# Kernel optimization log

Measured on AMD Instinct MI355X. Metric: run time of the kernel, lower is better.

## Reference

```python
import jax, jax.numpy as jnp
import numpy as np
import math

DIM = 2048
N_HEADS = 16
HEAD_DIM = 128
BATCH = 2
T = 2048
EPS = 1e-5


def setup_inputs() -> dict:
    key = jax.random.key(0)
    ks = jax.random.split(key, 16)
    s = lambda fan_in: 1.0 / math.sqrt(fan_in)
    d = {}
    d['x'] = jax.random.normal(ks[0], (BATCH, T, DIM), dtype=jnp.float32)
    d['start_pos'] = 0
    # attention projections (weights stored [in, out])
    d['wq'] = jax.random.uniform(ks[1], (DIM, N_HEADS * HEAD_DIM), minval=-s(DIM), maxval=s(DIM))
    d['bq'] = jnp.zeros((N_HEADS * HEAD_DIM,), jnp.float32)
    d['wk'] = jax.random.uniform(ks[2], (DIM, HEAD_DIM), minval=-s(DIM), maxval=s(DIM))
    d['bk'] = jnp.zeros((HEAD_DIM,), jnp.float32)
    d['wv'] = jax.random.uniform(ks[3], (DIM, HEAD_DIM), minval=-s(DIM), maxval=s(DIM))
    d['bv'] = jnp.zeros((HEAD_DIM,), jnp.float32)
    d['wo'] = jax.random.uniform(ks[4], (N_HEADS * HEAD_DIM, DIM), minval=-s(N_HEADS * HEAD_DIM), maxval=s(N_HEADS * HEAD_DIM))
    d['bo'] = jnp.zeros((DIM,), jnp.float32)
    # layernorms
    d['ln1_g'] = jnp.ones((DIM,), jnp.float32)
    d['ln1_b'] = jnp.zeros((DIM,), jnp.float32)
    d['ln2_g'] = jnp.ones((DIM,), jnp.float32)
    d['ln2_b'] = jnp.zeros((DIM,), jnp.float32)
    # MLP (dim -> 4*dim -> dim), dropout p=0 is a no-op
    d['w1'] = jax.random.uniform(ks[5], (DIM, 4 * DIM), minval=-s(DIM), maxval=s(DIM))
    d['b1'] = jnp.zeros((4 * DIM,), jnp.float32)
    d['w2'] = jax.random.uniform(ks[6], (4 * DIM, DIM), minval=-s(4 * DIM), maxval=s(4 * DIM))
    d['b2'] = jnp.zeros((DIM,), jnp.float32)
    return d


def _layernorm(h, g, b):
    mu = jnp.mean(h, axis=-1, keepdims=True)
    var = jnp.mean(jnp.square(h - mu), axis=-1, keepdims=True)
    return (h - mu) * jax.lax.rsqrt(var + EPS) * g + b


def reference(x, start_pos, wq, bq, wk, bk, wv, bv, wo, bo, ln1_g, ln1_b, ln2_g, ln2_b, w1, b1, w2, b2):
    B, Tq, D = x.shape
    hd = wk.shape[1]
    H = wq.shape[1] // hd
    # --- MQA attention on pre-LN input (prefill: no kv cache) ---
    h = _layernorm(x, ln1_g, ln1_b)
    q = (h @ wq + bq).reshape(B, Tq, H, hd)          # [B,T,H,hd]
    k = h @ wk + bk                                   # [B,T,hd] single shared head
    v = h @ wv + bv                                   # [B,T,hd]
    scores = jnp.einsum('bthc,bsc->bhts', q, k) / math.sqrt(hd)
    causal = jnp.where(jnp.tril(jnp.ones((Tq, Tq), dtype=bool)), 0.0, -jnp.inf).astype(scores.dtype)
    attn = jax.nn.softmax(scores + causal, axis=-1)   # [B,H,T,T]
    ctx = jnp.einsum('bhts,bsc->bthc', attn, v).reshape(B, Tq, H * hd)
    out = ctx @ wo + bo
    x = x + out
    # --- GELU MLP (exact erf gelu, torch default) ---
    h2 = _layernorm(x, ln2_g, ln2_b)
    x = x + jax.nn.gelu(h2 @ w1 + b1, approximate=False) @ w2 + b2
    k_cat = k[:, None]                                # [B,1,T,hd]
    v_cat = v[:, None]
    return (x, k_cat, v_cat)
```

## Files before the change

kernel.cpp:

```cpp
#include <hip/hip_runtime.h>
#include <stdint.h>

#define DIMSZ 2048
#define HD 128
#define NH 16
#define BATCH 2
#define SEQ 2048
#define MROWS (BATCH*SEQ)
#define FFDIM (4*DIMSZ)
#define NQKV (DIMSZ + 2*HD)

typedef float f32x4 __attribute__((ext_vector_type(4)));
typedef __bf16 bf16x8 __attribute__((ext_vector_type(8)));
typedef __bf16 bf16x2 __attribute__((ext_vector_type(2)));
typedef _Float16 f16x8 __attribute__((ext_vector_type(8)));
typedef __bf16 bf16_t;
typedef _Float16 f16_t;

__device__ __forceinline__ void async16(const void* g, void* l) {
  __builtin_amdgcn_global_load_lds(
      (const __attribute__((address_space(1))) void*)(uintptr_t)g,
      (__attribute__((address_space(3))) void*)(uint32_t)(uintptr_t)l,
      16, 0, 0);
}

__device__ __forceinline__ float gelu_f(float x) {
  return 0.5f * x * (1.0f + erff(x * 0.70710678118654752f));
}

__device__ __forceinline__ void hard_barrier() {
  asm volatile("" ::: "memory");
  __builtin_amdgcn_s_barrier();
  asm volatile("" ::: "memory");
}

__global__ __launch_bounds__(256)
void k_trall(const float* __restrict__ wq, const float* __restrict__ wk,
             const float* __restrict__ wv, const float* __restrict__ wo,
             const float* __restrict__ w1, const float* __restrict__ w2,
             bf16_t* __restrict__ wqkvT, bf16_t* __restrict__ woT,
             bf16_t* __restrict__ w1T, bf16_t* __restrict__ w2T) {
  int bid = blockIdx.x;
  const float* src; bf16_t* dst; int R, C, t0;
  if (bid < 1024)      { src = wq; dst = wqkvT;                        R = 2048; C = 2048; t0 = bid; }
  else if (bid < 1088) { src = wk; dst = wqkvT + (size_t)2048 * 2048;  R = 2048; C = 128;  t0 = bid - 1024; }
  else if (bid < 1152) { src = wv; dst = wqkvT + (size_t)2176 * 2048;  R = 2048; C = 128;  t0 = bid - 1088; }
  else if (bid < 2176) { src = wo; dst = woT;                          R = 2048; C = 2048; t0 = bid - 1152; }
  else if (bid < 6272) { src = w1; dst = w1T;                          R = 2048; C = 8192; t0 = bid - 2176; }
  else                 { src = w2; dst = w2T;                          R = 8192; C = 2048; t0 = bid - 6272; }
  int tc = C >> 6;
  int c0 = (t0 % tc) * 64, r0 = (t0 / tc) * 64;
  __shared__ float tile[64][65];
  int lc = threadIdx.x & 63, lrow = threadIdx.x >> 6;
#pragma unroll
  for (int i = 0; i < 64; i += 4)
    tile[lrow + i][lc] = src[(size_t)(r0 + lrow + i) * C + c0 + lc];
  __syncthreads();
  int rp = threadIdx.x & 31, wc = threadIdx.x >> 5;
#pragma unroll
  for (int i = 0; i < 64; i += 8) {
    int c = wc + i;
    bf16x2 pk = {(bf16_t)tile[2 * rp][c], (bf16_t)tile[2 * rp + 1][c]};
    *(bf16x2*)(dst + (size_t)(c0 + c) * R + r0 + 2 * rp) = pk;
  }
}

__global__ __launch_bounds__(256)
void k_transpose_v(const bf16_t* __restrict__ v, bf16_t* __restrict__ vt) {
  __shared__ bf16_t tile[32][33];
  int b = blockIdx.z;
  int t0 = blockIdx.x * 32, d0 = blockIdx.y * 32;
  int tx = threadIdx.x & 31, ty = threadIdx.x >> 5;
#pragma unroll
  for (int i = 0; i < 32; i += 8)
    tile[ty + i][tx] = v[((size_t)(b * SEQ + t0 + ty + i)) * HD + d0 + tx];
  __syncthreads();
#pragma unroll
  for (int i = 0; i < 32; i += 8)
    vt[((size_t)(b * HD + d0 + ty + i)) * SEQ + t0 + tx] = tile[tx][ty + i];
}

__global__ __launch_bounds__(256)
void k_layernorm(const float* __restrict__ x, const float* __restrict__ g,
                 const float* __restrict__ bb, bf16_t* __restrict__ out) {
  int row = blockIdx.x;
  const float* xr = x + (size_t)row * DIMSZ;
  int t = threadIdx.x;
  float vals[8];
  float s = 0.f, s2 = 0.f;
#pragma unroll
  for (int i = 0; i < 8; ++i) {
    float v = xr[t + i * 256];
    vals[i] = v; s += v; s2 += v * v;
  }
#pragma unroll
  for (int o = 1; o < 64; o <<= 1) { s += __shfl_xor(s, o); s2 += __shfl_xor(s2, o); }
  __shared__ float red[8];
  if ((t & 63) == 0) { red[t >> 6] = s; red[4 + (t >> 6)] = s2; }
  __syncthreads();
  s = red[0] + red[1] + red[2] + red[3];
  s2 = red[4] + red[5] + red[6] + red[7];
  float mu = s * (1.0f / DIMSZ);
  float rstd = rsqrtf(s2 * (1.0f / DIMSZ) - mu * mu + 1e-5f);
  bf16_t* orow = out + (size_t)row * DIMSZ;
#pragma unroll
  for (int i = 0; i < 8; ++i) {
    int c = t + i * 256;
    orow[c] = (bf16_t)((vals[i] - mu) * rstd * g[c] + bb[c]);
  }
}

template <int FN>
__device__ __forceinline__ void gemm8_loop(
    const bf16_t* __restrict__ A, const bf16_t* __restrict__ BT,
    int ld, int Kloop, int bm, int bn, f32x4 (&acc)[8][FN], bf16_t* sh) {
  constexpr int BH = FN >> 1;
  constexpr int BN = FN * 64;
  const int tid = threadIdx.x;
  const int lane = tid & 63, lr = lane & 15, lg = lane >> 4;
  const int wave = tid >> 6, wm = wave >> 2, wn = wave & 3;
  bf16_t* const Ab0 = sh;
  bf16_t* const Bb0 = sh + 32768;
  const bf16_t* const Ag = A + (size_t)bm * 256 * ld;
  const bf16_t* const Bg = BT + (size_t)bn * BN * ld;

  auto stage = [&](const bf16_t* gbase, bf16_t* lbase, int h, int t) {
#pragma unroll
    for (int j = 0; j < 2; ++j) {
      int flat = (tid + j * 512) * 8;
      int r = flat >> 6, kp = flat & 63;
      int ks = kp ^ ((r & 7) << 3);
      async16(gbase + (size_t)(h * 128 + r) * ld + t * 64 + ks, lbase + flat);
    }
  };
  auto stA = [&](int c, int h, int t) { stage(Ag, Ab0 + (c * 2 + h) * 8192, h, t); };
  auto stB = [&](int c, int h, int t) { stage(Bg, Bb0 + (c * BH + h) * 8192, h, t); };

  const int xsw = (lr & 7) << 3;
  bf16x8 a_[8], b_[FN][2];
  auto lda = [&](int c, int kk) {
    const bf16_t* base = Ab0 + (c * 2 + wm) * 8192;
#pragma unroll
    for (int mf = 0; mf < 8; ++mf)
      a_[mf] = *(const bf16x8*)(base + (mf * 16 + lr) * 64 + ((kk + lg * 8) ^ xsw));
  };
  auto ldb = [&](int c) {
#pragma unroll
    for (int nf = 0; nf < FN; ++nf) {
      int row = wn * (FN * 16) + nf * 16 + lr;
      const bf16_t* base =
          Bb0 + (c * BH + (BH == 2 ? (row >> 7) : 0)) * 8192 + (row & 127) * 64;
#pragma unroll
      for (int kx = 0; kx < 2; ++kx)
        b_[nf][kx] = *(const bf16x8*)(base + ((kx * 32 + lg * 8) ^ xsw));
    }
  };

#define LGKM0 asm volatile("s_waitcnt lgkmcnt(0)" ::: "memory");
#define VMC_STEADY                                                   \
  if (BH == 2) { asm volatile("s_waitcnt vmcnt(6)" ::: "memory"); }  \
  else         { asm volatile("s_waitcnt vmcnt(4)" ::: "memory"); }
#define MFMA_HALF(M0, KX)                                            \
  __builtin_amdgcn_s_setprio(1);                                     \
  _Pragma("unroll")                                                  \
  for (int mf = 0; mf < 4; ++mf)                                     \
    _Pragma("unroll")                                                \
    for (int nf = 0; nf < FN; ++nf)                                  \
      acc[(M0) + mf][nf] = __builtin_amdgcn_mfma_f32_16x16x32_bf16(  \
          a_[(M0) + mf], b_[nf][KX], acc[(M0) + mf][nf], 0, 0, 0);   \
  __builtin_amdgcn_s_setprio(0);

  const int nit = Kloop >> 7;

  stA(0, 0, 0); stA(0, 1, 0);
  stB(0, 0, 0); if (BH == 2) stB(0, 1, 0);
  stB(1, 0, 1); if (BH == 2) stB(1, 1, 1);
  stA(1, 0, 1);
  VMC_STEADY;
  hard_barrier();

  for (int i = 0; i < nit; ++i) {
    const int t1 = 2 * i + 1, t2 = 2 * i + 2, t3 = 2 * i + 3;
    const bool g2 = (i < nit - 1);
    lda(0, 0); ldb(0);
    stA(1, 1, t1);
    hard_barrier(); LGKM0;
    MFMA_HALF(0, 0)
    hard_barrier();
    if (g2) stB(0, 0, t2);
    hard_barrier();
    MFMA_HALF(4, 0)
    hard_barrier();
    lda(0, 32);
    if (g2 && BH == 2) stB(0, 1, t2);
    hard_barrier(); LGKM0;
    MFMA_HALF(0, 1)
    hard_barrier();
    if (g2) stA(0, 0, t2);
    if (i == nit - 1) { asm volatile("s_waitcnt vmcnt(0)" ::: "memory"); }
    else { VMC_STEADY; }
    hard_barrier();
    MFMA_HALF(4, 1)
    hard_barrier();
    lda(1, 0); ldb(1);
    if (g2) stA(0, 1, t2);
    hard_barrier(); LGKM0;
    MFMA_HALF(0, 0)
    hard_barrier();
    if (g2) stB(1, 0, t3);
    hard_barrier();
    MFMA_HALF(4, 0)
    hard_barrier();
    lda(1, 32);
    if (g2 && BH == 2) stB(1, 1, t3);
    hard_barrier(); LGKM0;
    MFMA_HALF(0, 1)
    hard_barrier();
    if (g2) {
      stA(1, 0, t3);
      VMC_STEADY;
    }
    hard_barrier();
    MFMA_HALF(4, 1)
    hard_barrier();
  }
#undef LGKM0
#undef VMC_STEADY
#undef MFMA_HALF
}

__global__ __launch_bounds__(512, 1)
void k_oproj(const bf16_t* __restrict__ A, const bf16_t* __restrict__ BT,
             const float* __restrict__ bias, const float* __restrict__ res,
             float* __restrict__ outF) {
  extern __shared__ __align__(16) bf16_t sh8[];
  const int nt = DIMSZ / 128;
  int bm = blockIdx.x / nt, bn = blockIdx.x % nt;
  f32x4 acc[8][2] = {};
  gemm8_loop<2>(A, BT, DIMSZ, DIMSZ, bm, bn, acc, sh8);
  int tid = threadIdx.x, wave = tid >> 6, lane = tid & 63, lr = lane & 15, lg = lane >> 4;
  int wm = wave >> 2, wn = wave & 3;
  float* shF = (float*)sh8;
  int rl0 = wm * 128 + lg * 4;
  int cl0 = wn * 32 + lr;
#pragma unroll
  for (int nf = 0; nf < 2; ++nf) {
    int cl = cl0 + nf * 16;
    float bi = bias[bn * 128 + cl];
#pragma unroll
    for (int mf = 0; mf < 8; ++mf)
#pragma unroll
      for (int j = 0; j < 4; ++j)
        shF[(rl0 + mf * 16 + j) * 128 + cl] = acc[mf][nf][j] + bi;
  }
  hard_barrier();
  const float* rbase = res + (size_t)(bm * 256) * DIMSZ + bn * 128;
  float* gbase = outF + (size_t)(bm * 256) * DIMSZ + bn * 128;
#pragma unroll
  for (int s = 0; s < 16; ++s) {
    int flat = s * 512 + tid;
    int row = flat >> 5, cu = flat & 31;
    f32x4 v = *(const f32x4*)(shF + row * 128 + cu * 4);
    f32x4 r4 = *(const f32x4*)(rbase + (size_t)row * DIMSZ + cu * 4);
    *(f32x4*)(gbase + (size_t)row * DIMSZ + cu * 4) = v + r4;
  }
}

__global__ __launch_bounds__(512, 1)
void k_ffn1(const bf16_t* __restrict__ A, const bf16_t* __restrict__ BT,
            const float* __restrict__ bias, bf16_t* __restrict__ outB) {
  extern __shared__ __align__(16) bf16_t sh8[];
  const int nt = FFDIM / 256;
  int bm = blockIdx.x / nt, bn = blockIdx.x % nt;
  f32x4 acc[8][4] = {};
  gemm8_loop<4>(A, BT, DIMSZ, DIMSZ, bm, bn, acc, sh8);
  int tid = threadIdx.x, wave = tid >> 6, lane = tid & 63, lr = lane & 15, lg = lane >> 4;
  int wm = wave >> 2, wn = wave & 3;
  int rl0 = wm * 128 + lg * 4;
  int cl0 = wn * 64 + lr;
#pragma unroll
  for (int nf = 0; nf < 4; ++nf) {
    int cl = cl0 + nf * 16;
    float bi = bias[bn * 256 + cl];
#pragma unroll
    for (int mf = 0; mf < 8; ++mf)
#pragma unroll
      for (int j = 0; j < 4; ++j)
        sh8[(rl0 + mf * 16 + j) * 256 + cl] = (bf16_t)gelu_f(acc[mf][nf][j] + bi);
  }
  hard_barrier();
  bf16_t* gbase = outB + (size_t)(bm * 256) * FFDIM + bn * 256;
#pragma unroll
  for (int s = 0; s < 16; ++s) {
    int flat = s * 512 + tid;
    int row = flat >> 5, cu = flat & 31;
    f32x4 v = *(const f32x4*)(sh8 + row * 256 + cu * 8);
    *(f32x4*)(gbase + (size_t)row * FFDIM + cu * 8) = v;
  }
}

__global__ __launch_bounds__(512, 1)
void k_ffn2(const bf16_t* __restrict__ A, const bf16_t* __restrict__ BT,
            f16_t* __restrict__ p0, f16_t* __restrict__ p1) {
  extern __shared__ __align__(16) bf16_t sh8[];
  int swz = (blockIdx.x & 7) * 32 + (blockIdx.x >> 3);
  int kh = swz >> 7;
  int tile = swz & 127;
  int bm = tile >> 3, bn = tile & 7;
  f32x4 acc[8][4] = {};
  gemm8_loop<4>(A + kh * (FFDIM / 2), BT + kh * (FFDIM / 2), FFDIM, FFDIM / 2,
                bm, bn, acc, sh8);
  int tid = threadIdx.x, wave = tid >> 6, lane = tid & 63, lr = lane & 15, lg = lane >> 4;
  int wm = wave >> 2, wn = wave & 3;
  f16_t* shH = (f16_t*)sh8;
  int rl0 = wm * 128 + lg * 4;
  int cl0 = wn * 64 + lr;
#pragma unroll
  for (int nf = 0; nf < 4; ++nf) {
    int cl = cl0 + nf * 16;
#pragma unroll
    for (int mf = 0; mf < 8; ++mf)
#pragma unroll
      for (int j = 0; j < 4; ++j)
        shH[(rl0 + mf * 16 + j) * 256 + cl] = (f16_t)acc[mf][nf][j];
  }
  hard_barrier();
  f16_t* gbase = (kh ? p1 : p0) + (size_t)(bm * 256) * DIMSZ + bn * 256;
#pragma unroll
  for (int s = 0; s < 16; ++s) {
    int flat = s * 512 + tid;
    int row = flat >> 5, cu = flat & 31;
    f32x4 v = *(const f32x4*)(shH + row * 256 + cu * 8);
    *(f32x4*)(gbase + (size_t)row * DIMSZ + cu * 8) = v;
  }
}

__global__ __launch_bounds__(256)
void k_ffn2red(const f16_t* __restrict__ p0, const f16_t* __restrict__ p1,
               const float* __restrict__ b2, float* __restrict__ outx) {
  int row = blockIdx.x;
  int c0 = threadIdx.x * 8;
  size_t base = (size_t)row * DIMSZ + c0;
  f16x8 a = *(const f16x8*)(p0 + base);
  f16x8 b = *(const f16x8*)(p1 + base);
  f32x4 o0 = *(const f32x4*)(outx + base);
  f32x4 o1 = *(const f32x4*)(outx + base + 4);
  f32x4 b0 = *(const f32x4*)(b2 + c0);
  f32x4 b1 = *(const f32x4*)(b2 + c0 + 4);
#pragma unroll
  for (int i = 0; i < 4; ++i) {
    o0[i] += (float)a[i] + (float)b[i] + b0[i];
    o1[i] += (float)a[4 + i] + (float)b[4 + i] + b1[i];
  }
  *(f32x4*)(outx + base) = o0;
  *(f32x4*)(outx + base + 4) = o1;
}

__global__ __launch_bounds__(512, 1)
void k_qkv(const bf16_t* __restrict__ A, const bf16_t* __restrict__ BT,
           const float* __restrict__ bq, const float* __restrict__ bk,
           const float* __restrict__ bv,
           bf16_t* __restrict__ qb, float* __restrict__ outk,
           float* __restrict__ outv, bf16_t* __restrict__ kbf,
           bf16_t* __restrict__ vbf) {
  extern __shared__ __align__(16) bf16_t sh8[];
  const int nt = NQKV / 256;
  int bm = blockIdx.x / nt, bn = blockIdx.x % nt;
  f32x4 acc[8][4] = {};
  gemm8_loop<4>(A, BT, DIMSZ, DIMSZ, bm, bn, acc, sh8);
  int tid = threadIdx.x, wave = tid >> 6, lane = tid & 63, lr = lane & 15, lg = lane >> 4;
  int wm = wave >> 2, wn = wave & 3;
  int rl0 = wm * 128 + lg * 4;
  int cl0 = wn * 64 + lr;
#pragma unroll
  for (int nf = 0; nf < 4; ++nf) {
    int cl = cl0 + nf * 16;
    int cg = bn * 256 + cl;
    float bi = (cg < 2048) ? bq[cg] : (cg < 2176 ? bk[cg - 2048] : bv[cg - 2176]);
#pragma unroll
    for (int mf = 0; mf < 8; ++mf)
#pragma unroll
      for (int j = 0; j < 4; ++j) {
        float v = acc[mf][nf][j] + bi;
        sh8[(rl0 + mf * 16 + j) * 256 + cl] = (bf16_t)v;
        if (cg >= 2048) {
          int r = bm * 256 + rl0 + mf * 16 + j;
          if (cg < 2176) outk[(size_t)r * HD + (cg - 2048)] = v;
          else           outv[(size_t)r * HD + (cg - 2176)] = v;
        }
      }
  }
  hard_barrier();
#pragma unroll
  for (int s = 0; s < 16; ++s) {
    int flat = s * 512 + tid;
    int row = flat >> 5, cu = flat & 31;
    f32x4 v = *(const f32x4*)(sh8 + row * 256 + cu * 8);
    int r = bm * 256 + row;
    if (bn < 8) {
      *(f32x4*)(qb + (size_t)r * DIMSZ + bn * 256 + cu * 8) = v;
    } else {
      int ce = cu * 8;
      if (ce < 128) *(f32x4*)(kbf + (size_t)r * HD + ce) = v;
      else          *(f32x4*)(vbf + (size_t)r * HD + (ce - 128)) = v;
    }
  }
}

__global__ __launch_bounds__(256, 2)
void k_attn(const bf16_t* __restrict__ q, const bf16_t* __restrict__ k,
            const bf16_t* __restrict__ vt, bf16_t* __restrict__ ctx) {
  __shared__ __align__(16) bf16_t Ks[2][64 * 128];
  __shared__ __align__(16) bf16_t Vs[2][128 * 64];
  __shared__ bf16_t Pw[4][16][72];
  int pp = blockIdx.x, h = blockIdx.y, b = blockIdx.z;
  int tid = threadIdx.x, wave = tid >> 6, lane = tid & 63, lr = lane & 15, lg = lane >> 4;
  const bf16_t* kb = k + (size_t)b * SEQ * HD;
  const bf16_t* vb = vt + (size_t)b * HD * SEQ;

#define STAGE_TILE(buf, s0_)                                                      \
  {                                                                               \
    _Pragma("unroll")                                                             \
    for (int i = 0; i < 4; ++i) {                                                 \
      int flat = (i * 256 + tid) * 8;                                             \
      int kr = flat >> 7, kc = flat & 127;                                        \
      int ksrc = (((kc >> 3) ^ (kr & 7)) << 3) | (kc & 7);                        \
      async16(kb + (size_t)((s0_) + kr) * HD + ksrc, (void*)(Ks[buf] + flat));    \
      int vr = flat >> 6, vc = flat & 63;                                         \
      int vsrc = (((vc >> 3) ^ (vr & 7)) << 3) | (vc & 7);                        \
      async16(vb + (size_t)vr * SEQ + (s0_) + vsrc, (void*)(Vs[buf] + flat));     \
    }                                                                             \
  }

  for (int half = 0; half < 2; ++half) {
    int qt = half ? (31 - pp) : pp;
    int q0 = qt * 64;
    int qw = q0 + wave * 16;
    const bf16_t* qbase = q + ((size_t)(b * SEQ + qw + lr)) * DIMSZ + h * HD;
    bf16x8 qf[4];
#pragma unroll
    for (int kk = 0; kk < 4; ++kk) qf[kk] = *(const bf16x8*)(qbase + kk * 32 + lg * 8);
    f32x4 o[8] = {};
    float m_[4], l_[4];
#pragma unroll
    for (int j = 0; j < 4; ++j) { m_[j] = -3.0e38f; l_[j] = 0.f; }
    int qglob0 = qw + lg * 4;
    int ntiles = qt + 1;

    STAGE_TILE(0, 0)
    __syncthreads();
    for (int t = 0; t < ntiles; ++t) {
      int cur = t & 1;
      if (t + 1 < ntiles) STAGE_TILE(cur ^ 1, (t + 1) * 64)
      int s0 = t * 64;
      const bf16_t* Kc = Ks[cur];
      const bf16_t* Vc = Vs[cur];
      f32x4 sf[4] = {};
#pragma unroll
      for (int nf = 0; nf < 4; ++nf) {
        int R = nf * 16 + lr;
#pragma unroll
        for (int kk = 0; kk < 4; ++kk)
          sf[nf] = __builtin_amdgcn_mfma_f32_16x16x32_bf16(
              qf[kk],
              *(const bf16x8*)(Kc + R * 128 + (((kk * 4 + lg) ^ (R & 7)) << 3)),
              sf[nf], 0, 0, 0);
      }
#pragma unroll
      for (int nf = 0; nf < 4; ++nf) {
        int col = s0 + nf * 16 + lr;
#pragma unroll
        for (int j = 0; j < 4; ++j) {
          float v = sf[nf][j] * 0.088388347648318447f;
          sf[nf][j] = (col <= qglob0 + j) ? v : -3.0e38f;
        }
      }
      float mx[4];
#pragma unroll
      for (int j = 0; j < 4; ++j)
        mx[j] = fmaxf(fmaxf(sf[0][j], sf[1][j]), fmaxf(sf[2][j], sf[3][j]));
#pragma unroll
      for (int o_ = 1; o_ < 16; o_ <<= 1)
#pragma unroll
        for (int j = 0; j < 4; ++j) mx[j] = fmaxf(mx[j], __shfl_xor(mx[j], o_));
      float fsc[4], mn[4];
#pragma unroll
      for (int j = 0; j < 4; ++j) {
        mn[j] = fmaxf(m_[j], mx[j]);
        fsc[j] = __expf(m_[j] - mn[j]);
        m_[j] = mn[j];
      }
      float ps[4] = {0.f, 0.f, 0.f, 0.f};
#pragma unroll
      for (int nf = 0; nf < 4; ++nf)
#pragma unroll
        for (int j = 0; j < 4; ++j) {
          float pv = __expf(sf[nf][j] - mn[j]);
          ps[j] += pv;
          Pw[wave][lg * 4 + j][nf * 16 + lr] = (bf16_t)pv;
        }
#pragma unroll
      for (int o_ = 1; o_ < 16; o_ <<= 1)
#pragma unroll
        for (int j = 0; j < 4; ++j) ps[j] += __shfl_xor(ps[j], o_);
#pragma unroll
      for (int j = 0; j < 4; ++j) l_[j] = l_[j] * fsc[j] + ps[j];
#pragma unroll
      for (int df = 0; df < 8; ++df)
#pragma unroll
        for (int j = 0; j < 4; ++j) o[df][j] *= fsc[j];
      asm volatile("" ::: "memory");
      bf16x8 pa[2];
#pragma unroll
      for (int kk = 0; kk < 2; ++kk)
        pa[kk] = *(const bf16x8*)(&Pw[wave][lr][kk * 32 + lg * 8]);
#pragma unroll
      for (int df = 0; df < 8; ++df) {
        int R = df * 16 + lr;
#pragma unroll
        for (int kk = 0; kk < 2; ++kk)
          o[df] = __builtin_amdgcn_mfma_f32_16x16x32_bf16(
              pa[kk],
              *(const bf16x8*)(Vc + R * 64 + (((kk * 4 + lg) ^ (R & 7)) << 3)),
              o[df], 0, 0, 0);
      }
      __syncthreads();
    }
    bf16_t* cb = ctx + ((size_t)(b * SEQ + qw)) * DIMSZ + h * HD;
#pragma unroll
    for (int df = 0; df < 8; ++df)
#pragma unroll
      for (int j = 0; j < 4; ++j)
        cb[(size_t)(lg * 4 + j) * DIMSZ + df * 16 + lr] = (bf16_t)(o[df][j] / l_[j]);
  }
#undef STAGE_TILE
}

extern "C" void kernel_launch(void* const* d_in, const int* in_sizes, int n_in,
                              void* d_out, int out_size, void* d_ws, size_t ws_size,
                              hipStream_t stream) {
  const float* x   = (const float*)d_in[0];
  const float* wq  = (const float*)d_in[2];
  const float* bq  = (const float*)d_in[3];
  const float* wk  = (const float*)d_in[4];
  const float* bk  = (const float*)d_in[5];
  const float* wv  = (const float*)d_in[6];
  const float* bv  = (const float*)d_in[7];
  const float* wo  = (const float*)d_in[8];
  const float* bo  = (const float*)d_in[9];
  const float* g1  = (const float*)d_in[10];
  const float* be1 = (const float*)d_in[11];
  const float* g2  = (const float*)d_in[12];
  const float* be2 = (const float*)d_in[13];
  const float* w1  = (const float*)d_in[14];
  const float* bb1 = (const float*)d_in[15];
  const float* w2  = (const float*)d_in[16];
  const float* bb2 = (const float*)d_in[17];

  float* outx = (float*)d_out;
  float* outk = outx + (size_t)MROWS * DIMSZ;
  float* outv = outk + (size_t)MROWS * HD;

  char* p = (char*)d_ws;
  auto alloc = [&](size_t bytes) -> char* {
    char* r = p;
    p += (bytes + 255) & ~(size_t)255;
    return r;
  };
  bf16_t* wqkvT = (bf16_t*)alloc((size_t)NQKV * DIMSZ * 2);
  bf16_t* woT = (bf16_t*)alloc((size_t)DIMSZ * DIMSZ * 2);
  bf16_t* w1T = (bf16_t*)alloc((size_t)FFDIM * DIMSZ * 2);
  bf16_t* w2T = (bf16_t*)alloc((size_t)DIMSZ * FFDIM * 2);
  bf16_t* hb  = (bf16_t*)alloc((size_t)MROWS * DIMSZ * 2);
  bf16_t* qb  = (bf16_t*)alloc((size_t)MROWS * DIMSZ * 2);
  bf16_t* kbf = (bf16_t*)alloc((size_t)MROWS * HD * 2);
  bf16_t* vbf = (bf16_t*)alloc((size_t)MROWS * HD * 2);
  bf16_t* vtb = (bf16_t*)alloc((size_t)BATCH * HD * SEQ * 2);
  bf16_t* f1b = (bf16_t*)alloc((size_t)MROWS * FFDIM * 2);
  f16_t* p0  = (f16_t*)alloc((size_t)MROWS * DIMSZ * 2);
  f16_t* p1  = (f16_t*)alloc((size_t)MROWS * DIMSZ * 2);
  (void)ws_size; (void)in_sizes; (void)n_in; (void)out_size;

  dim3 blk(256);
  const int LDSG = 131072;
  k_trall<<<10368, blk, 0, stream>>>(wq, wk, wv, wo, w1, w2, wqkvT, woT, w1T, w2T);
  k_layernorm<<<MROWS, blk, 0, stream>>>(x, g1, be1, hb);
  k_qkv<<<(MROWS / 256) * (NQKV / 256), 512, LDSG, stream>>>(
      hb, wqkvT, bq, bk, bv, qb, outk, outv, kbf, vbf);
  k_transpose_v<<<dim3(SEQ / 32, HD / 32, BATCH), blk, 0, stream>>>(vbf, vtb);
  k_attn<<<dim3(SEQ / 64 / 2, NH, BATCH), blk, 0, stream>>>(qb, kbf, vtb, hb);
  k_oproj<<<(MROWS / 256) * (DIMSZ / 128), 512, LDSG, stream>>>(hb, woT, bo, x, outx);
  k_layernorm<<<MROWS, blk, 0, stream>>>(outx, g2, be2, qb);
  k_ffn1<<<(MROWS / 256) * (FFDIM / 256), 512, LDSG, stream>>>(qb, w1T, bb1, f1b);
  k_ffn2<<<256, 512, LDSG, stream>>>(f1b, w2T, p0, p1);
  k_ffn2red<<<MROWS, blk, 0, stream>>>(p0, p1, bb2, outx);
}
```

Measured before the change: 523.0 us.

## Split A/B fragment loads into quarters and restage global prefetch schedule

The GEMM main loop now loads A fragments four at a time and B fragments one k-half at a time before each MFMA quarter, instead of holding eight A fragments and both B halves at once. This cuts the register footprint. The global-to-LDS staging is regrouped so both A halves, and both B halves, are issued together, with vmcnt thresholds lowered to match. The trade is more LDS read phases, each followed by an lgkmcnt wait and extra barriers inside the loop, which could expose LDS latency.

```diff
diff --git a/kernel.cpp b/kernel.cpp
--- a/kernel.cpp
+++ b/kernel.cpp
@@ -137,37 +137,35 @@
   auto stB = [&](int c, int h, int t) { stage(Bg, Bb0 + (c * BH + h) * 8192, h, t); };
 
   const int xsw = (lr & 7) << 3;
-  bf16x8 a_[8], b_[FN][2];
-  auto lda = [&](int c, int kk) {
+  bf16x8 a_[4], b_[FN][2];
+  auto lda4 = [&](int c, int m0, int kk) {
     const bf16_t* base = Ab0 + (c * 2 + wm) * 8192;
 #pragma unroll
-    for (int mf = 0; mf < 8; ++mf)
-      a_[mf] = *(const bf16x8*)(base + (mf * 16 + lr) * 64 + ((kk + lg * 8) ^ xsw));
+    for (int i = 0; i < 4; ++i)
+      a_[i] = *(const bf16x8*)(base + ((m0 + i) * 16 + lr) * 64 + ((kk + lg * 8) ^ xsw));
   };
-  auto ldb = [&](int c) {
+  auto ldb4 = [&](int c, int kx) {
 #pragma unroll
     for (int nf = 0; nf < FN; ++nf) {
       int row = wn * (FN * 16) + nf * 16 + lr;
       const bf16_t* base =
           Bb0 + (c * BH + (BH == 2 ? (row >> 7) : 0)) * 8192 + (row & 127) * 64;
-#pragma unroll
-      for (int kx = 0; kx < 2; ++kx)
-        b_[nf][kx] = *(const bf16x8*)(base + ((kx * 32 + lg * 8) ^ xsw));
+      b_[nf][kx] = *(const bf16x8*)(base + ((kx * 32 + lg * 8) ^ xsw));
     }
   };
 
 #define LGKM0 asm volatile("s_waitcnt lgkmcnt(0)" ::: "memory");
-#define VMC_STEADY                                                   \
-  if (BH == 2) { asm volatile("s_waitcnt vmcnt(6)" ::: "memory"); }  \
-  else         { asm volatile("s_waitcnt vmcnt(4)" ::: "memory"); }
-#define MFMA_HALF(M0, KX)                                            \
+#define VMC_GATE                                                     \
+  if (BH == 2) { asm volatile("s_waitcnt vmcnt(4)" ::: "memory"); }  \
+  else         { asm volatile("s_waitcnt vmcnt(2)" ::: "memory"); }
+#define MFMA_Q(M0, KX)                                               \
   __builtin_amdgcn_s_setprio(1);                                     \
   _Pragma("unroll")                                                  \
-  for (int mf = 0; mf < 4; ++mf)                                     \
+  for (int i_ = 0; i_ < 4; ++i_)                                     \
     _Pragma("unroll")                                                \
     for (int nf = 0; nf < FN; ++nf)                                  \
-      acc[(M0) + mf][nf] = __builtin_amdgcn_mfma_f32_16x16x32_bf16(  \
-          a_[(M0) + mf], b_[nf][KX], acc[(M0) + mf][nf], 0, 0, 0);   \
+      acc[(M0) + i_][nf] = __builtin_amdgcn_mfma_f32_16x16x32_bf16(  \
+          a_[i_], b_[nf][KX], acc[(M0) + i_][nf], 0, 0, 0);          \
   __builtin_amdgcn_s_setprio(0);
 
   const int nit = Kloop >> 7;
@@ -175,58 +173,55 @@
   stA(0, 0, 0); stA(0, 1, 0);
   stB(0, 0, 0); if (BH == 2) stB(0, 1, 0);
   stB(1, 0, 1); if (BH == 2) stB(1, 1, 1);
-  stA(1, 0, 1);
-  VMC_STEADY;
+  VMC_GATE;
   hard_barrier();
 
   for (int i = 0; i < nit; ++i) {
     const int t1 = 2 * i + 1, t2 = 2 * i + 2, t3 = 2 * i + 3;
     const bool g2 = (i < nit - 1);
-    lda(0, 0); ldb(0);
-    stA(1, 1, t1);
-    hard_barrier(); LGKM0;
-    MFMA_HALF(0, 0)
-    hard_barrier();
-    if (g2) stB(0, 0, t2);
-    hard_barrier();
-    MFMA_HALF(4, 0)
-    hard_barrier();
-    lda(0, 32);
-    if (g2 && BH == 2) stB(0, 1, t2);
-    hard_barrier(); LGKM0;
-    MFMA_HALF(0, 1)
-    hard_barrier();
-    if (g2) stA(0, 0, t2);
+    lda4(0, 0, 0); ldb4(0, 0);
+    stA(1, 0, t1); stA(1, 1, t1);
+    hard_barrier(); LGKM0;
+    MFMA_Q(0, 0)
+    hard_barrier();
+    lda4(0, 4, 0); ldb4(0, 1);
+    hard_barrier(); LGKM0;
+    MFMA_Q(4, 0)
+    hard_barrier();
+    lda4(0, 0, 32);
+    if (g2) { stB(0, 0, t2); if (BH == 2) stB(0, 1, t2); }
+    hard_barrier(); LGKM0;
+    MFMA_Q(0, 1)
+    hard_barrier();
+    lda4(0, 4, 32);
     if (i == nit - 1) { asm volatile("s_waitcnt vmcnt(0)" ::: "memory"); }
-    else { VMC_STEADY; }
-    hard_barrier();
-    MFMA_HALF(4, 1)
-    hard_barrier();
-    lda(1, 0); ldb(1);
-    if (g2) stA(0, 1, t2);
-    hard_barrier(); LGKM0;
-    MFMA_HALF(0, 0)
-    hard_barrier();
-    if (g2) stB(1, 0, t3);
-    hard_barrier();
-    MFMA_HALF(4, 0)
-    hard_barrier();
-    lda(1, 32);
-    if (g2 && BH == 2) stB(1, 1, t3);
-    hard_barrier(); LGKM0;
-    MFMA_HALF(0, 1)
-    hard_barrier();
-    if (g2) {
-      stA(1, 0, t3);
-      VMC_STEADY;
-    }
-    hard_barrier();
-    MFMA_HALF(4, 1)
+    else { VMC_GATE; }
+    hard_barrier(); LGKM0;
+    MFMA_Q(4, 1)
+    hard_barrier();
+    lda4(1, 0, 0); ldb4(1, 0);
+    if (g2) { stA(0, 0, t2); stA(0, 1, t2); }
+    hard_barrier(); LGKM0;
+    MFMA_Q(0, 0)
+    hard_barrier();
+    lda4(1, 4, 0); ldb4(1, 1);
+    hard_barrier(); LGKM0;
+    MFMA_Q(4, 0)
+    hard_barrier();
+    lda4(1, 0, 32);
+    if (g2) { stB(1, 0, t3); if (BH == 2) stB(1, 1, t3); }
+    hard_barrier(); LGKM0;
+    MFMA_Q(0, 1)
+    hard_barrier();
+    lda4(1, 4, 32);
+    VMC_GATE;
+    hard_barrier(); LGKM0;
+    MFMA_Q(4, 1)
     hard_barrier();
   }
 #undef LGKM0
-#undef VMC_STEADY
-#undef MFMA_HALF
+#undef VMC_GATE
+#undef MFMA_Q
 }
 
 __global__ __launch_bounds__(512, 1)
```

New measurement: 527.4 us. About the same (+0.8%).

## Switch shared GEMM loop from 16x16x32 to 32x32x16 bf16 MFMA tiles

Applied to the files above, without the earlier changes.

Rewrites the common GEMM mainloop and all its epilogues to use 32x32x16 bf16 MFMA instructions with f32x16 accumulators instead of 16x16x32 with f32x4. The LDS fragment loads, K-slot indexing and the accumulator-to-row mapping in the epilogues are reworked to match. Larger MFMA tiles cut the number of LDS fragment reads per FLOP and the instruction issue count. The cost is a different register layout and epilogue scatter pattern, which can cause LDS bank conflicts or raise register pressure.

```diff
diff --git a/kernel.cpp b/kernel.cpp
--- a/kernel.cpp
+++ b/kernel.cpp
@@ -11,6 +11,7 @@
 #define NQKV (DIMSZ + 2*HD)
 
 typedef float f32x4 __attribute__((ext_vector_type(4)));
+typedef float f32x16 __attribute__((ext_vector_type(16)));
 typedef __bf16 bf16x8 __attribute__((ext_vector_type(8)));
 typedef __bf16 bf16x2 __attribute__((ext_vector_type(2)));
 typedef _Float16 f16x8 __attribute__((ext_vector_type(8)));
@@ -113,11 +114,12 @@
 template <int FN>
 __device__ __forceinline__ void gemm8_loop(
     const bf16_t* __restrict__ A, const bf16_t* __restrict__ BT,
-    int ld, int Kloop, int bm, int bn, f32x4 (&acc)[8][FN], bf16_t* sh) {
+    int ld, int Kloop, int bm, int bn, f32x16 (&acc)[4][(FN >> 1)], bf16_t* sh) {
   constexpr int BH = FN >> 1;
   constexpr int BN = FN * 64;
+  constexpr int NF = FN >> 1;
   const int tid = threadIdx.x;
-  const int lane = tid & 63, lr = lane & 15, lg = lane >> 4;
+  const int lane = tid & 63, l31 = lane & 31, hi = lane >> 5;
   const int wave = tid >> 6, wm = wave >> 2, wn = wave & 3;
   bf16_t* const Ab0 = sh;
   bf16_t* const Bb0 = sh + 32768;
@@ -136,23 +138,26 @@
   auto stA = [&](int c, int h, int t) { stage(Ag, Ab0 + (c * 2 + h) * 8192, h, t); };
   auto stB = [&](int c, int h, int t) { stage(Bg, Bb0 + (c * BH + h) * 8192, h, t); };
 
-  const int xsw = (lr & 7) << 3;
-  bf16x8 a_[8], b_[FN][2];
-  auto lda = [&](int c, int kk) {
+  const int xsw = (l31 & 7) << 3;
+  bf16x8 a_[8], b_[NF][4];
+  auto lda = [&](int c, int kslot) {
     const bf16_t* base = Ab0 + (c * 2 + wm) * 8192;
 #pragma unroll
-    for (int mf = 0; mf < 8; ++mf)
-      a_[mf] = *(const bf16x8*)(base + (mf * 16 + lr) * 64 + ((kk + lg * 8) ^ xsw));
+    for (int mf = 0; mf < 4; ++mf)
+#pragma unroll
+      for (int kh = 0; kh < 2; ++kh)
+        a_[mf * 2 + kh] = *(const bf16x8*)(base + (mf * 32 + l31) * 64 +
+                           ((((kslot * 2 + kh) * 16) + hi * 8) ^ xsw));
   };
   auto ldb = [&](int c) {
 #pragma unroll
-    for (int nf = 0; nf < FN; ++nf) {
-      int row = wn * (FN * 16) + nf * 16 + lr;
+    for (int nf = 0; nf < NF; ++nf) {
+      int row = wn * (NF * 32) + nf * 32 + l31;
       const bf16_t* base =
           Bb0 + (c * BH + (BH == 2 ? (row >> 7) : 0)) * 8192 + (row & 127) * 64;
 #pragma unroll
-      for (int kx = 0; kx < 2; ++kx)
-        b_[nf][kx] = *(const bf16x8*)(base + ((kx * 32 + lg * 8) ^ xsw));
+      for (int ks = 0; ks < 4; ++ks)
+        b_[nf][ks] = *(const bf16x8*)(base + ((ks * 16 + hi * 8) ^ xsw));
     }
   };
 
@@ -160,14 +165,17 @@
 #define VMC_STEADY                                                   \
   if (BH == 2) { asm volatile("s_waitcnt vmcnt(6)" ::: "memory"); }  \
   else         { asm volatile("s_waitcnt vmcnt(4)" ::: "memory"); }
-#define MFMA_HALF(M0, KX)                                            \
+#define MFMA_HALF(MH, KSL)                                           \
   __builtin_amdgcn_s_setprio(1);                                     \
   _Pragma("unroll")                                                  \
-  for (int mf = 0; mf < 4; ++mf)                                     \
+  for (int m2 = 0; m2 < 2; ++m2)                                     \
     _Pragma("unroll")                                                \
-    for (int nf = 0; nf < FN; ++nf)                                  \
-      acc[(M0) + mf][nf] = __builtin_amdgcn_mfma_f32_16x16x32_bf16(  \
-          a_[(M0) + mf], b_[nf][KX], acc[(M0) + mf][nf], 0, 0, 0);   \
+    for (int kh = 0; kh < 2; ++kh)                                   \
+      _Pragma("unroll")                                              \
+      for (int nf = 0; nf < NF; ++nf)                                \
+        acc[(MH) * 2 + m2][nf] = __builtin_amdgcn_mfma_f32_32x32x16_bf16( \
+            a_[((MH) * 2 + m2) * 2 + kh], b_[nf][(KSL) * 2 + kh],    \
+            acc[(MH) * 2 + m2][nf], 0, 0, 0);                        \
   __builtin_amdgcn_s_setprio(0);
 
   const int nit = Kloop >> 7;
@@ -189,9 +197,9 @@
     hard_barrier();
     if (g2) stB(0, 0, t2);
     hard_barrier();
-    MFMA_HALF(4, 0)
-    hard_barrier();
-    lda(0, 32);
+    MFMA_HALF(1, 0)
+    hard_barrier();
+    lda(0, 1);
     if (g2 && BH == 2) stB(0, 1, t2);
     hard_barrier(); LGKM0;
     MFMA_HALF(0, 1)
@@ -200,7 +208,7 @@
     if (i == nit - 1) { asm volatile("s_waitcnt vmcnt(0)" ::: "memory"); }
     else { VMC_STEADY; }
     hard_barrier();
-    MFMA_HALF(4, 1)
+    MFMA_HALF(1, 1)
     hard_barrier();
     lda(1, 0); ldb(1);
     if (g2) stA(0, 1, t2);
@@ -209,9 +217,9 @@
     hard_barrier();
     if (g2) stB(1, 0, t3);
     hard_barrier();
-    MFMA_HALF(4, 0)
-    hard_barrier();
-    lda(1, 32);
+    MFMA_HALF(1, 0)
+    hard_barrier();
+    lda(1, 1);
     if (g2 && BH == 2) stB(1, 1, t3);
     hard_barrier(); LGKM0;
     MFMA_HALF(0, 1)
@@ -221,13 +229,14 @@
       VMC_STEADY;
     }
     hard_barrier();
-    MFMA_HALF(4, 1)
+    MFMA_HALF(1, 1)
     hard_barrier();
   }
 #undef LGKM0
 #undef VMC_STEADY
 #undef MFMA_HALF
 }
+
 
 __global__ __launch_bounds__(512, 1)
 void k_oproj(const bf16_t* __restrict__ A, const bf16_t* __restrict__ BT,
@@ -236,23 +245,20 @@
   extern __shared__ __align__(16) bf16_t sh8[];
   const int nt = DIMSZ / 128;
   int bm = blockIdx.x / nt, bn = blockIdx.x % nt;
-  f32x4 acc[8][2] = {};
+  f32x16 acc[4][1] = {};
   gemm8_loop<2>(A, BT, DIMSZ, DIMSZ, bm, bn, acc, sh8);
-  int tid = threadIdx.x, wave = tid >> 6, lane = tid & 63, lr = lane & 15, lg = lane >> 4;
+  int tid = threadIdx.x, wave = tid >> 6, lane = tid & 63, l31 = lane & 31, hi = lane >> 5;
   int wm = wave >> 2, wn = wave & 3;
   float* shF = (float*)sh8;
-  int rl0 = wm * 128 + lg * 4;
-  int cl0 = wn * 32 + lr;
-#pragma unroll
-  for (int nf = 0; nf < 2; ++nf) {
-    int cl = cl0 + nf * 16;
-    float bi = bias[bn * 128 + cl];
-#pragma unroll
-    for (int mf = 0; mf < 8; ++mf)
-#pragma unroll
-      for (int j = 0; j < 4; ++j)
-        shF[(rl0 + mf * 16 + j) * 128 + cl] = acc[mf][nf][j] + bi;
-  }
+  int cl = wn * 32 + l31;
+  float bi = bias[bn * 128 + cl];
+#pragma unroll
+  for (int mf = 0; mf < 4; ++mf)
+#pragma unroll
+    for (int r16 = 0; r16 < 16; ++r16) {
+      int rl = wm * 128 + mf * 32 + (r16 & 3) + ((r16 >> 2) << 3) + hi * 4;
+      shF[rl * 128 + cl] = acc[mf][0][r16] + bi;
+    }
   hard_barrier();
   const float* rbase = res + (size_t)(bm * 256) * DIMSZ + bn * 128;
   float* gbase = outF + (size_t)(bm * 256) * DIMSZ + bn * 128;
@@ -272,21 +278,21 @@
   extern __shared__ __align__(16) bf16_t sh8[];
   const int nt = FFDIM / 256;
   int bm = blockIdx.x / nt, bn = blockIdx.x % nt;
-  f32x4 acc[8][4] = {};
+  f32x16 acc[4][2] = {};
   gemm8_loop<4>(A, BT, DIMSZ, DIMSZ, bm, bn, acc, sh8);
-  int tid = threadIdx.x, wave = tid >> 6, lane = tid & 63, lr = lane & 15, lg = lane >> 4;
+  int tid = threadIdx.x, wave = tid >> 6, lane = tid & 63, l31 = lane & 31, hi = lane >> 5;
   int wm = wave >> 2, wn = wave & 3;
-  int rl0 = wm * 128 + lg * 4;
-  int cl0 = wn * 64 + lr;
-#pragma unroll
-  for (int nf = 0; nf < 4; ++nf) {
-    int cl = cl0 + nf * 16;
+#pragma unroll
+  for (int nf = 0; nf < 2; ++nf) {
+    int cl = wn * 64 + nf * 32 + l31;
     float bi = bias[bn * 256 + cl];
 #pragma unroll
-    for (int mf = 0; mf < 8; ++mf)
-#pragma unroll
-      for (int j = 0; j < 4; ++j)
-        sh8[(rl0 + mf * 16 + j) * 256 + cl] = (bf16_t)gelu_f(acc[mf][nf][j] + bi);
+    for (int mf = 0; mf < 4; ++mf)
+#pragma unroll
+      for (int r16 = 0; r16 < 16; ++r16) {
+        int rl = wm * 128 + mf * 32 + (r16 & 3) + ((r16 >> 2) << 3) + hi * 4;
+        sh8[rl * 256 + cl] = (bf16_t)gelu_f(acc[mf][nf][r16] + bi);
+      }
   }
   hard_barrier();
   bf16_t* gbase = outB + (size_t)(bm * 256) * FFDIM + bn * 256;
@@ -307,22 +313,22 @@
   int kh = swz >> 7;
   int tile = swz & 127;
   int bm = tile >> 3, bn = tile & 7;
-  f32x4 acc[8][4] = {};
+  f32x16 acc[4][2] = {};
   gemm8_loop<4>(A + kh * (FFDIM / 2), BT + kh * (FFDIM / 2), FFDIM, FFDIM / 2,
                 bm, bn, acc, sh8);
-  int tid = threadIdx.x, wave = tid >> 6, lane = tid & 63, lr = lane & 15, lg = lane >> 4;
+  int tid = threadIdx.x, wave = tid >> 6, lane = tid & 63, l31 = lane & 31, hi = lane >> 5;
   int wm = wave >> 2, wn = wave & 3;
   f16_t* shH = (f16_t*)sh8;
-  int rl0 = wm * 128 + lg * 4;
-  int cl0 = wn * 64 + lr;
-#pragma unroll
-  for (int nf = 0; nf < 4; ++nf) {
-    int cl = cl0 + nf * 16;
-#pragma unroll
-    for (int mf = 0; mf < 8; ++mf)
-#pragma unroll
-      for (int j = 0; j < 4; ++j)
-        shH[(rl0 + mf * 16 + j) * 256 + cl] = (f16_t)acc[mf][nf][j];
+#pragma unroll
+  for (int nf = 0; nf < 2; ++nf) {
+    int cl = wn * 64 + nf * 32 + l31;
+#pragma unroll
+    for (int mf = 0; mf < 4; ++mf)
+#pragma unroll
+      for (int r16 = 0; r16 < 16; ++r16) {
+        int rl = wm * 128 + mf * 32 + (r16 & 3) + ((r16 >> 2) << 3) + hi * 4;
+        shH[rl * 256 + cl] = (f16_t)acc[mf][nf][r16];
+      }
   }
   hard_barrier();
   f16_t* gbase = (kh ? p1 : p0) + (size_t)(bm * 256) * DIMSZ + bn * 256;
@@ -366,25 +372,24 @@
   extern __shared__ __align__(16) bf16_t sh8[];
   const int nt = NQKV / 256;
   int bm = blockIdx.x / nt, bn = blockIdx.x % nt;
-  f32x4 acc[8][4] = {};
+  f32x16 acc[4][2] = {};
   gemm8_loop<4>(A, BT, DIMSZ, DIMSZ, bm, bn, acc, sh8);
-  int tid = threadIdx.x, wave = tid >> 6, lane = tid & 63, lr = lane & 15, lg = lane >> 4;
+  int tid = threadIdx.x, wave = tid >> 6, lane = tid & 63, l31 = lane & 31, hi = lane >> 5;
   int wm = wave >> 2, wn = wave & 3;
-  int rl0 = wm * 128 + lg * 4;
-  int cl0 = wn * 64 + lr;
-#pragma unroll
-  for (int nf = 0; nf < 4; ++nf) {
-    int cl = cl0 + nf * 16;
+#pragma unroll
+  for (int nf = 0; nf < 2; ++nf) {
+    int cl = wn * 64 + nf * 32 + l31;
     int cg = bn * 256 + cl;
     float bi = (cg < 2048) ? bq[cg] : (cg < 2176 ? bk[cg - 2048] : bv[cg - 2176]);
 #pragma unroll
-    for (int mf = 0; mf < 8; ++mf)
-#pragma unroll
-      for (int j = 0; j < 4; ++j) {
-        float v = acc[mf][nf][j] + bi;
-        sh8[(rl0 + mf * 16 + j) * 256 + cl] = (bf16_t)v;
+    for (int mf = 0; mf < 4; ++mf)
+#pragma unroll
+      for (int r16 = 0; r16 < 16; ++r16) {
+        int rl = wm * 128 + mf * 32 + (r16 & 3) + ((r16 >> 2) << 3) + hi * 4;
+        float v = acc[mf][nf][r16] + bi;
+        sh8[rl * 256 + cl] = (bf16_t)v;
         if (cg >= 2048) {
-          int r = bm * 256 + rl0 + mf * 16 + j;
+          int r = bm * 256 + rl;
           if (cg < 2176) outk[(size_t)r * HD + (cg - 2048)] = v;
           else           outv[(size_t)r * HD + (cg - 2176)] = v;
         }
```

New measurement: 568.7 us. 1.09x slower.
